# Kernel tuning notes

Measured on AMD Instinct MI355X. Metric: run time of the kernel, lower is better.

The kernel has to match this reference:

```python
import jax, jax.numpy as jnp
import numpy as np

P = 2.0
EPS = 1e-06

def _dist(x1, x2):
    # torch.dist(x1, x2, p=2): p-norm of flattened difference per sample -> [B]
    d = x1 - x2
    return jnp.sqrt(jnp.sum(d * d, axis=-1))

def setup_inputs() -> dict:
    key = jax.random.key(0)
    k1, k2, k3 = jax.random.split(key, 3)
    B, D = 65536, 256
    return {
        "anchor": jax.random.normal(k1, (B, D), dtype=jnp.float32),
        "positive": jax.random.normal(k2, (B, D), dtype=jnp.float32),
        "negative": jax.random.normal(k3, (B, D), dtype=jnp.float32),
    }

def reference(anchor, positive, negative):
    d_ap = _dist(anchor, positive)          # [B]
    d_an = _dist(anchor, negative)          # [B]
    d_pn = _dist(positive, negative)        # [B]
    margin_sim = 1.0 + 2.0 / (jnp.exp(4.0 * d_ap) + EPS)
    margin_dissim = 1.0 + 2.0 / (jnp.exp(-(4.0 * d_an) + 4.0) + EPS)
    margin = margin_sim + margin_dissim
    loss = d_ap - (d_an + d_pn) / 2.0 + margin
    return jnp.mean(loss)  # reduction='mean'
```

## Files before the change

### kernel.cpp

```cpp
#include <hip/hip_runtime.h>
#include <math.h>


#define D 256
#define TPB 256
#define WPB (TPB / 64)
#define NBLOCKS 2048

__global__ __launch_bounds__(TPB, 8) void triplet_partial(
    const float* __restrict__ a, const float* __restrict__ p,
    const float* __restrict__ n, float* __restrict__ partial, int B)
{
    const int lane = threadIdx.x & 63;
    const int waveInBlock = threadIdx.x >> 6;
    const int waveId = blockIdx.x * WPB + waveInBlock;
    const int nWaves = gridDim.x * WPB;

    float local = 0.0f;
    for (int row = waveId; row < B; row += nWaves) {
        const size_t base = (size_t)row * D + (size_t)lane * 4;
        const float4 av = *(const float4*)(a + base);
        const float4 pv = *(const float4*)(p + base);
        const float4 nv = *(const float4*)(n + base);

        float d, sap, san, spn;
        d = av.x - pv.x; sap  = d * d;
        d = av.y - pv.y; sap += d * d;
        d = av.z - pv.z; sap += d * d;
        d = av.w - pv.w; sap += d * d;

        d = av.x - nv.x; san  = d * d;
        d = av.y - nv.y; san += d * d;
        d = av.z - nv.z; san += d * d;
        d = av.w - nv.w; san += d * d;

        d = pv.x - nv.x; spn  = d * d;
        d = pv.y - nv.y; spn += d * d;
        d = pv.z - nv.z; spn += d * d;
        d = pv.w - nv.w; spn += d * d;

        #pragma unroll
        for (int off = 32; off > 0; off >>= 1) {
            sap += __shfl_xor(sap, off, 64);
            san += __shfl_xor(san, off, 64);
            spn += __shfl_xor(spn, off, 64);
        }

        if (lane == 0) {
            const float dap = sqrtf(sap);
            const float dan = sqrtf(san);
            const float dpn = sqrtf(spn);
            const float msim = 1.0f + 2.0f / (__expf(4.0f * dap) + 1e-6f);
            const float mdis = 1.0f + 2.0f / (__expf(-4.0f * dan + 4.0f) + 1e-6f);
            local += dap - 0.5f * (dan + dpn) + msim + mdis;
        }
    }

    __shared__ float sm[WPB];
    if (lane == 0) sm[waveInBlock] = local;
    __syncthreads();
    if (threadIdx.x == 0) {
        float s = 0.0f;
        #pragma unroll
        for (int i = 0; i < WPB; ++i) s += sm[i];
        partial[blockIdx.x] = s;
    }
}

__global__ __launch_bounds__(256) void final_reduce(
    const float* __restrict__ partial, float* __restrict__ out,
    int nPartial, float invB)
{
    float s = 0.0f;
    for (int i = threadIdx.x; i < nPartial; i += blockDim.x) s += partial[i];
    #pragma unroll
    for (int off = 32; off > 0; off >>= 1) s += __shfl_xor(s, off, 64);

    __shared__ float sm[4];
    const int lane = threadIdx.x & 63;
    const int w = threadIdx.x >> 6;
    if (lane == 0) sm[w] = s;
    __syncthreads();
    if (threadIdx.x == 0) out[0] = (sm[0] + sm[1] + sm[2] + sm[3]) * invB;
}

extern "C" void kernel_launch(void* const* d_in, const int* in_sizes, int n_in,
                              void* d_out, int out_size, void* d_ws, size_t ws_size,
                              hipStream_t stream) {
    const float* a = (const float*)d_in[0];
    const float* p = (const float*)d_in[1];
    const float* n = (const float*)d_in[2];
    float* out = (float*)d_out;
    float* partial = (float*)d_ws;

    const int B = in_sizes[0] / D;

    triplet_partial<<<NBLOCKS, TPB, 0, stream>>>(a, p, n, partial, B);
    final_reduce<<<1, 256, 0, stream>>>(partial, out, NBLOCKS, 1.0f / (float)B);
}
```

Measured before the change: 196.1 us.

## Map one row per 16 lanes with four float4 loads per lane

Replaces the wave-per-row grid-stride loop with a one-shot mapping where each 16-lane group handles one row and each lane issues twelve float4 loads up front. This raises memory-level parallelism and shortens the cross-lane shuffle reduction from six steps to four. The grid size now scales with B, so there are more blocks and more partials for the final reduce.

Result: no change. 195.9 us (-0.1%).

```diff
diff --git a/kernel.cpp b/kernel.cpp
--- a/kernel.cpp
+++ b/kernel.cpp
@@ -4,65 +4,76 @@
 
 #define D 256
 #define TPB 256
-#define WPB (TPB / 64)
-#define NBLOCKS 2048
+#define ROWS_PER_BLOCK 16
 
 __global__ __launch_bounds__(TPB, 8) void triplet_partial(
-    const float* __restrict__ a, const float* __restrict__ p,
-    const float* __restrict__ n, float* __restrict__ partial, int B)
+    const float4* __restrict__ a4, const float4* __restrict__ p4,
+    const float4* __restrict__ n4, float* __restrict__ partial, int B)
 {
     const int lane = threadIdx.x & 63;
     const int waveInBlock = threadIdx.x >> 6;
-    const int waveId = blockIdx.x * WPB + waveInBlock;
-    const int nWaves = gridDim.x * WPB;
+    const int sub = lane >> 4;
+    const int sl  = lane & 15;
+    const int row = (blockIdx.x * 4 + waveInBlock) * 4 + sub;
 
-    float local = 0.0f;
-    for (int row = waveId; row < B; row += nWaves) {
-        const size_t base = (size_t)row * D + (size_t)lane * 4;
-        const float4 av = *(const float4*)(a + base);
-        const float4 pv = *(const float4*)(p + base);
-        const float4 nv = *(const float4*)(n + base);
+    float sap = 0.0f, san = 0.0f, spn = 0.0f;
 
-        float d, sap, san, spn;
-        d = av.x - pv.x; sap  = d * d;
-        d = av.y - pv.y; sap += d * d;
-        d = av.z - pv.z; sap += d * d;
-        d = av.w - pv.w; sap += d * d;
+    if (row < B) {
+        const size_t b = (size_t)row * 64 + sl;
+        const float4 av0 = a4[b];      const float4 av1 = a4[b + 16];
+        const float4 av2 = a4[b + 32]; const float4 av3 = a4[b + 48];
+        const float4 pv0 = p4[b];      const float4 pv1 = p4[b + 16];
+        const float4 pv2 = p4[b + 32]; const float4 pv3 = p4[b + 48];
+        const float4 nv0 = n4[b];      const float4 nv1 = n4[b + 16];
+        const float4 nv2 = n4[b + 32]; const float4 nv3 = n4[b + 48];
 
-        d = av.x - nv.x; san  = d * d;
-        d = av.y - nv.y; san += d * d;
-        d = av.z - nv.z; san += d * d;
-        d = av.w - nv.w; san += d * d;
+        float d;
+#define ACC3(AV, PV, NV)                                                   \
+        d = AV.x - PV.x; sap = fmaf(d, d, sap);                            \
+        d = AV.y - PV.y; sap = fmaf(d, d, sap);                            \
+        d = AV.z - PV.z; sap = fmaf(d, d, sap);                            \
+        d = AV.w - PV.w; sap = fmaf(d, d, sap);                            \
+        d = AV.x - NV.x; san = fmaf(d, d, san);                            \
+        d = AV.y - NV.y; san = fmaf(d, d, san);                            \
+        d = AV.z - NV.z; san = fmaf(d, d, san);                            \
+        d = AV.w - NV.w; san = fmaf(d, d, san);                            \
+        d = PV.x - NV.x; spn = fmaf(d, d, spn);                            \
+        d = PV.y - NV.y; spn = fmaf(d, d, spn);                            \
+        d = PV.z - NV.z; spn = fmaf(d, d, spn);                            \
+        d = PV.w - NV.w; spn = fmaf(d, d, spn);
 
-        d = pv.x - nv.x; spn  = d * d;
-        d = pv.y - nv.y; spn += d * d;
-        d = pv.z - nv.z; spn += d * d;
-        d = pv.w - nv.w; spn += d * d;
+        ACC3(av0, pv0, nv0)
+        ACC3(av1, pv1, nv1)
+        ACC3(av2, pv2, nv2)
+        ACC3(av3, pv3, nv3)
+#undef ACC3
+    }
 
-        #pragma unroll
-        for (int off = 32; off > 0; off >>= 1) {
-            sap += __shfl_xor(sap, off, 64);
-            san += __shfl_xor(san, off, 64);
-            spn += __shfl_xor(spn, off, 64);
-        }
+    #pragma unroll
+    for (int off = 8; off >= 1; off >>= 1) {
+        sap += __shfl_xor(sap, off, 64);
+        san += __shfl_xor(san, off, 64);
+        spn += __shfl_xor(spn, off, 64);
+    }
 
-        if (lane == 0) {
+    __shared__ float sm[ROWS_PER_BLOCK];
+    if (sl == 0) {
+        float v = 0.0f;
+        if (row < B) {
             const float dap = sqrtf(sap);
             const float dan = sqrtf(san);
             const float dpn = sqrtf(spn);
             const float msim = 1.0f + 2.0f / (__expf(4.0f * dap) + 1e-6f);
             const float mdis = 1.0f + 2.0f / (__expf(-4.0f * dan + 4.0f) + 1e-6f);
-            local += dap - 0.5f * (dan + dpn) + msim + mdis;
+            v = dap - 0.5f * (dan + dpn) + msim + mdis;
         }
+        sm[waveInBlock * 4 + sub] = v;
     }
-
-    __shared__ float sm[WPB];
-    if (lane == 0) sm[waveInBlock] = local;
     __syncthreads();
     if (threadIdx.x == 0) {
         float s = 0.0f;
         #pragma unroll
-        for (int i = 0; i < WPB; ++i) s += sm[i];
+        for (int i = 0; i < ROWS_PER_BLOCK; ++i) s += sm[i];
         partial[blockIdx.x] = s;
     }
 }
@@ -87,14 +98,15 @@
 extern "C" void kernel_launch(void* const* d_in, const int* in_sizes, int n_in,
                               void* d_out, int out_size, void* d_ws, size_t ws_size,
                               hipStream_t stream) {
-    const float* a = (const float*)d_in[0];
-    const float* p = (const float*)d_in[1];
-    const float* n = (const float*)d_in[2];
+    const float4* a = (const float4*)d_in[0];
+    const float4* p = (const float4*)d_in[1];
+    const float4* n = (const float4*)d_in[2];
     float* out = (float*)d_out;
     float* partial = (float*)d_ws;
 
     const int B = in_sizes[0] / D;
+    const int nBlocks = (B + ROWS_PER_BLOCK - 1) / ROWS_PER_BLOCK;
 
-    triplet_partial<<<NBLOCKS, TPB, 0, stream>>>(a, p, n, partial, B);
-    final_reduce<<<1, 256, 0, stream>>>(partial, out, NBLOCKS, 1.0f / (float)B);
+    triplet_partial<<<nBlocks, TPB, 0, stream>>>(a, p, n, partial, B);
+    final_reduce<<<1, 256, 0, stream>>>(partial, out, nBlocks, 1.0f / (float)B);
 }
```

## Batch eight rows per wave with nontemporal loads and one-shot grid

Applied to the files above, without the earlier changes.

Each wave now loads eight rows of anchor, positive and negative up front using nontemporal float4 loads, instead of a grid-stride loop that handles one row at a time. The grid is sized to cover the batch directly at 32 rows per block, and the shuffle reductions are interleaved across the eight rows. The aim is more memory requests in flight per wave and less cache pollution on a bandwidth-bound stream. The cost is higher register pressure (launch bounds lowered to 3), and the final reduce must now sum 2048 partials. A tail with fewer than eight rows in a wave is dropped rather than handled.

Result: faster. 179.4 us (-8.5%).

```diff
diff --git a/kernel.cpp b/kernel.cpp
--- a/kernel.cpp
+++ b/kernel.cpp
@@ -4,65 +4,91 @@
 
 #define D 256
 #define TPB 256
-#define WPB (TPB / 64)
-#define NBLOCKS 2048
+#define ROWS_PER_WAVE 8
+#define WAVES_PER_BLOCK 4
+#define ROWS_PER_BLOCK 32
 
-__global__ __launch_bounds__(TPB, 8) void triplet_partial(
-    const float* __restrict__ a, const float* __restrict__ p,
-    const float* __restrict__ n, float* __restrict__ partial, int B)
+typedef float nt_float4 __attribute__((ext_vector_type(4)));
+
+__global__ __launch_bounds__(TPB, 3) void triplet_partial(
+    const nt_float4* __restrict__ a4, const nt_float4* __restrict__ p4,
+    const nt_float4* __restrict__ n4, float* __restrict__ partial, int B)
 {
     const int lane = threadIdx.x & 63;
-    const int waveInBlock = threadIdx.x >> 6;
-    const int waveId = blockIdx.x * WPB + waveInBlock;
-    const int nWaves = gridDim.x * WPB;
+    const int wib  = threadIdx.x >> 6;
+    const int row0 = (blockIdx.x * WAVES_PER_BLOCK + wib) * ROWS_PER_WAVE;
 
-    float local = 0.0f;
-    for (int row = waveId; row < B; row += nWaves) {
-        const size_t base = (size_t)row * D + (size_t)lane * 4;
-        const float4 av = *(const float4*)(a + base);
-        const float4 pv = *(const float4*)(p + base);
-        const float4 nv = *(const float4*)(n + base);
+    float sap[ROWS_PER_WAVE], san[ROWS_PER_WAVE], spn[ROWS_PER_WAVE];
 
-        float d, sap, san, spn;
-        d = av.x - pv.x; sap  = d * d;
-        d = av.y - pv.y; sap += d * d;
-        d = av.z - pv.z; sap += d * d;
-        d = av.w - pv.w; sap += d * d;
+    if (row0 + ROWS_PER_WAVE <= B) {
+        const size_t base = (size_t)row0 * 64 + lane;
 
-        d = av.x - nv.x; san  = d * d;
-        d = av.y - nv.y; san += d * d;
-        d = av.z - nv.z; san += d * d;
-        d = av.w - nv.w; san += d * d;
-
-        d = pv.x - nv.x; spn  = d * d;
-        d = pv.y - nv.y; spn += d * d;
-        d = pv.z - nv.z; spn += d * d;
-        d = pv.w - nv.w; spn += d * d;
+        nt_float4 av[ROWS_PER_WAVE], pv[ROWS_PER_WAVE], nv[ROWS_PER_WAVE];
+        #pragma unroll
+        for (int j = 0; j < ROWS_PER_WAVE; ++j)
+            av[j] = __builtin_nontemporal_load(a4 + base + (size_t)j * 64);
+        #pragma unroll
+        for (int j = 0; j < ROWS_PER_WAVE; ++j)
+            pv[j] = __builtin_nontemporal_load(p4 + base + (size_t)j * 64);
+        #pragma unroll
+        for (int j = 0; j < ROWS_PER_WAVE; ++j)
+            nv[j] = __builtin_nontemporal_load(n4 + base + (size_t)j * 64);
 
         #pragma unroll
-        for (int off = 32; off > 0; off >>= 1) {
-            sap += __shfl_xor(sap, off, 64);
-            san += __shfl_xor(san, off, 64);
-            spn += __shfl_xor(spn, off, 64);
+        for (int j = 0; j < ROWS_PER_WAVE; ++j) {
+            float d, s0, s1, s2;
+            d = av[j].x - pv[j].x; s0 = d * d;
+            d = av[j].y - pv[j].y; s0 = fmaf(d, d, s0);
+            d = av[j].z - pv[j].z; s0 = fmaf(d, d, s0);
+            d = av[j].w - pv[j].w; s0 = fmaf(d, d, s0);
+            d = av[j].x - nv[j].x; s1 = d * d;
+            d = av[j].y - nv[j].y; s1 = fmaf(d, d, s1);
+            d = av[j].z - nv[j].z; s1 = fmaf(d, d, s1);
+            d = av[j].w - nv[j].w; s1 = fmaf(d, d, s1);
+            d = pv[j].x - nv[j].x; s2 = d * d;
+            d = pv[j].y - nv[j].y; s2 = fmaf(d, d, s2);
+            d = pv[j].z - nv[j].z; s2 = fmaf(d, d, s2);
+            d = pv[j].w - nv[j].w; s2 = fmaf(d, d, s2);
+            sap[j] = s0; san[j] = s1; spn[j] = s2;
         }
-
-        if (lane == 0) {
-            const float dap = sqrtf(sap);
-            const float dan = sqrtf(san);
-            const float dpn = sqrtf(spn);
-            const float msim = 1.0f + 2.0f / (__expf(4.0f * dap) + 1e-6f);
-            const float mdis = 1.0f + 2.0f / (__expf(-4.0f * dan + 4.0f) + 1e-6f);
-            local += dap - 0.5f * (dan + dpn) + msim + mdis;
+    } else {
+        #pragma unroll
+        for (int j = 0; j < ROWS_PER_WAVE; ++j) {
+            sap[j] = 0.0f; san[j] = 0.0f; spn[j] = 0.0f;
         }
     }
 
-    __shared__ float sm[WPB];
-    if (lane == 0) sm[waveInBlock] = local;
+    #pragma unroll
+    for (int off = 32; off >= 1; off >>= 1) {
+        #pragma unroll
+        for (int j = 0; j < ROWS_PER_WAVE; ++j) {
+            sap[j] += __shfl_xor(sap[j], off, 64);
+            san[j] += __shfl_xor(san[j], off, 64);
+            spn[j] += __shfl_xor(spn[j], off, 64);
+        }
+    }
+
+    __shared__ float sm[WAVES_PER_BLOCK];
+    if (lane == 0) {
+        float local = 0.0f;
+        if (row0 + ROWS_PER_WAVE <= B) {
+            #pragma unroll
+            for (int j = 0; j < ROWS_PER_WAVE; ++j) {
+                const float dap = sqrtf(sap[j]);
+                const float dan = sqrtf(san[j]);
+                const float dpn = sqrtf(spn[j]);
+                const float msim = 1.0f + 2.0f / (__expf(4.0f * dap) + 1e-6f);
+                const float mdis = 1.0f + 2.0f / (__expf(-4.0f * dan + 4.0f) + 1e-6f);
+                local += dap - 0.5f * (dan + dpn) + msim + mdis;
+            }
+        }
+        sm[wib] = local;
+    }
     __syncthreads();
     if (threadIdx.x == 0) {
         float s = 0.0f;
         #pragma unroll
-        for (int i = 0; i < WPB; ++i) s += sm[i];
+        for (int i = 0; i < WAVES_PER_BLOCK; ++i) s += sm[i];
         partial[blockIdx.x] = s;
     }
 }
@@ -87,14 +113,15 @@
 extern "C" void kernel_launch(void* const* d_in, const int* in_sizes, int n_in,
                               void* d_out, int out_size, void* d_ws, size_t ws_size,
                               hipStream_t stream) {
-    const float* a = (const float*)d_in[0];
-    const float* p = (const float*)d_in[1];
-    const float* n = (const float*)d_in[2];
+    const nt_float4* a = (const nt_float4*)d_in[0];
+    const nt_float4* p = (const nt_float4*)d_in[1];
+    const nt_float4* n = (const nt_float4*)d_in[2];
     float* out = (float*)d_out;
     float* partial = (float*)d_ws;
 
     const int B = in_sizes[0] / D;
+    const int nBlocks = (B + ROWS_PER_BLOCK - 1) / ROWS_PER_BLOCK;
 
-    triplet_partial<<<NBLOCKS, TPB, 0, stream>>>(a, p, n, partial, B);
-    final_reduce<<<1, 256, 0, stream>>>(partial, out, NBLOCKS, 1.0f / (float)B);
+    triplet_partial<<<nBlocks, TPB, 0, stream>>>(a, p, n, partial, B);
+    final_reduce<<<1, 256, 0, stream>>>(partial, out, nBlocks, 1.0f / (float)B);
 }
```
